# Kernel optimization log

Measured on AMD Instinct MI355X. Metric: run time of the kernel, lower is better.

Reference implementation:

```python
import jax, jax.numpy as jnp
import numpy as np

B = 65536
IN1, IN2 = 384, 128
GRU1, GRU2, NLEVELS = 384, 16, 256


def gru_step(x, h, kernel, rkernel, bias):
    """Single Keras GRU (reset_after=True) step. Gate order: z, r, h.
    kernel: [in, 3u], rkernel: [u, 3u], bias: [2, 3u] (input bias, recurrent bias)."""
    u = h.shape[-1]
    xi = x @ kernel + bias[0]          # [B, 3u]
    hr = h @ rkernel + bias[1]         # [B, 3u]
    xz, xr, xh = xi[:, :u], xi[:, u:2 * u], xi[:, 2 * u:]
    hz, hrr, hh = hr[:, :u], hr[:, u:2 * u], hr[:, 2 * u:]
    z = jax.nn.sigmoid(xz + hz)
    r = jax.nn.sigmoid(xr + hrr)
    hcand = jnp.tanh(xh + r * hh)
    return z * h + (1.0 - z) * hcand


def setup_inputs() -> dict:
    key = jax.random.key(0)
    ks = jax.random.split(key, 14)
    s = lambda fan: 1.0 / np.sqrt(fan)
    return {
        "x1": jax.random.normal(ks[0], (B, IN1), jnp.float32),
        "x2": jax.random.normal(ks[1], (B, IN2), jnp.float32),
        "gru1_kernel": jax.random.normal(ks[2], (IN1 + IN2, 3 * GRU1), jnp.float32) * s(IN1 + IN2),
        "gru1_rkernel": jax.random.normal(ks[3], (GRU1, 3 * GRU1), jnp.float32) * s(GRU1),
        "gru1_bias": jax.random.normal(ks[4], (2, 3 * GRU1), jnp.float32) * 0.01,
        "gru2_kernel": jax.random.normal(ks[5], (GRU1, 3 * GRU2), jnp.float32) * s(GRU1),
        "gru2_rkernel": jax.random.normal(ks[6], (GRU2, 3 * GRU2), jnp.float32) * s(GRU2),
        "gru2_bias": jax.random.normal(ks[7], (2, 3 * GRU2), jnp.float32) * 0.01,
        "fc_w1": jax.random.normal(ks[8], (GRU2, NLEVELS), jnp.float32) * s(GRU2),
        "fc_b1": jax.random.normal(ks[9], (NLEVELS,), jnp.float32) * 0.01,
        "fc_w2": jax.random.normal(ks[10], (GRU2, NLEVELS), jnp.float32) * s(GRU2),
        "fc_b2": jax.random.normal(ks[11], (NLEVELS,), jnp.float32) * 0.01,
        "fc_g1": jax.random.normal(ks[12], (NLEVELS,), jnp.float32),
        "fc_g2": jax.random.normal(ks[13], (NLEVELS,), jnp.float32),
    }


def reference(x1, x2, gru1_kernel, gru1_rkernel, gru1_bias,
              gru2_kernel, gru2_rkernel, gru2_bias,
              fc_w1, fc_b1, fc_w2, fc_b2, fc_g1, fc_g2):
    e = jnp.concatenate([x1, x2], axis=-1)                      # [B, 512]
    h1 = gru_step(e, jnp.zeros((e.shape[0], GRU1), e.dtype),
                  gru1_kernel, gru1_rkernel, gru1_bias)         # [B, 384]
    h2 = gru_step(h1, jnp.zeros((e.shape[0], GRU2), e.dtype),
                  gru2_kernel, gru2_rkernel, gru2_bias)         # [B, 16]
    # DualFC (LPCNet): weighted sum of two tanh branches
    d = fc_g1 * jnp.tanh(h2 @ fc_w1 + fc_b1) + fc_g2 * jnp.tanh(h2 @ fc_w2 + fc_b2)
    return jax.nn.softmax(d, axis=-1)                           # [B, 256]
```

## Files before the change

### kernel.cpp

```cpp
#include <hip/hip_runtime.h>

typedef unsigned short u16;
typedef unsigned int   u32;
typedef float f32x4 __attribute__((ext_vector_type(4)));
typedef short s16x8 __attribute__((ext_vector_type(8)));

#define NB    65536
#define K1    512
#define N1    1152
#define G1D   384
#define K2    384
#define G2D   16
#define NL    256

__device__ inline u16 f2bf(float f) {
  u32 u = __float_as_uint(f);
  u += 0x7fffu + ((u >> 16) & 1u);
  return (u16)(u >> 16);
}
__device__ inline float bf2f(u16 h) { return __uint_as_float(((u32)h) << 16); }
__device__ inline float sigmoidf_(float x) { return 1.0f / (1.0f + __expf(-x)); }
__device__ inline float tanhf_(float x) {
  float e = __expf(2.0f * fabsf(x));
  float t = 1.0f - 2.0f / (e + 1.0f);
  return copysignf(t, x);
}

__device__ inline void gld16(const u16* g, u16* l) {
  __builtin_amdgcn_global_load_lds(
      (const __attribute__((address_space(1))) void*)g,
      (__attribute__((address_space(3))) void*)l, 16, 0, 0);
}

__global__ void prep_a(const float* __restrict__ x1, const float* __restrict__ x2,
                       u16* __restrict__ Abf) {
  int t = blockIdx.x * 256 + threadIdx.x;
  int i = t * 8;
  int row = i >> 9, col = i & 511;
  const float* src = (col < 384) ? (x1 + row * 384 + col) : (x2 + row * 128 + (col - 384));
  float4 v0 = ((const float4*)src)[0];
  float4 v1 = ((const float4*)src)[1];
  union { uint4 v; u16 u[8]; } o;
  o.u[0] = f2bf(v0.x); o.u[1] = f2bf(v0.y); o.u[2] = f2bf(v0.z); o.u[3] = f2bf(v0.w);
  o.u[4] = f2bf(v1.x); o.u[5] = f2bf(v1.y); o.u[6] = f2bf(v1.z); o.u[7] = f2bf(v1.w);
  *(uint4*)(Abf + i) = o.v;
}

__global__ __launch_bounds__(256) void prep_wt1(const float* __restrict__ w,
                                                u16* __restrict__ wt) {
  __shared__ float tile[64][65];
  const int nt = blockIdx.x * 64;
  const int kt = blockIdx.y * 64;
  const int tr = threadIdx.x >> 4;
  const int tc = (threadIdx.x & 15) * 4;
#pragma unroll
  for (int p = 0; p < 4; p++) {
    int k = kt + p * 16 + tr;
    float4 v = *(const float4*)(w + (long)k * N1 + nt + tc);
    tile[p * 16 + tr][tc + 0] = v.x;
    tile[p * 16 + tr][tc + 1] = v.y;
    tile[p * 16 + tr][tc + 2] = v.z;
    tile[p * 16 + tr][tc + 3] = v.w;
  }
  __syncthreads();
  const int nl = threadIdx.x >> 3;
  const int kc = (threadIdx.x & 7) * 8;
#pragma unroll
  for (int p = 0; p < 2; p++) {
    int n = nl + p * 32;
    union { uint4 v; u16 u[8]; } o;
#pragma unroll
    for (int j = 0; j < 8; j++) o.u[j] = f2bf(tile[kc + j][n]);
    *(uint4*)(wt + (long)(nt + n) * K1 + kt + kc) = o.v;
  }
}

__global__ void prep_wt(const float* __restrict__ w, u16* __restrict__ wt, int K, int N) {
  int n = blockIdx.x;
  int k0 = threadIdx.x * 8;
  if (k0 >= K) return;
  union { uint4 v; u16 u[8]; } o;
#pragma unroll
  for (int j = 0; j < 8; j++) o.u[j] = f2bf(w[(k0 + j) * N + n]);
  *(uint4*)(wt + n * K + k0) = o.v;
}

__global__ __launch_bounds__(256) void gemm1gate(const u16* __restrict__ A,
                                                 const u16* __restrict__ Bt,
                                                 const float* __restrict__ bias,
                                                 u16* __restrict__ H1) {
  __shared__ u16 As[128 * 32];
  __shared__ u16 Bs[3][64 * 32];
  const int tid = threadIdx.x;
  const int wave = tid >> 6, lane = tid & 63;
  const int quad = lane >> 4, l16 = lane & 15;

  const int id = blockIdx.x;
  const int xcd = id & 7;
  const int s = id >> 3;
  const int sd6 = s / 6;
  const int ublk = s - sd6 * 6;
  const int mbase = (xcd * 64 + sd6) * 128;
  const int ucbase = ublk * 64;

  const int wm = (wave & 1) * 64, wu = (wave >> 1) * 32;

  f32x4 acc[3][4][2];
#pragma unroll
  for (int g = 0; g < 3; g++)
#pragma unroll
    for (int i = 0; i < 4; i++)
#pragma unroll
      for (int j = 0; j < 2; j++)
#pragma unroll
        for (int r = 0; r < 4; r++) acc[g][i][j][r] = 0.0f;

  const int r0 = tid >> 2;
  const int kcg = ((tid & 3) ^ ((r0 >> 1) & 3)) * 8;
  const u16* Aptr = A + (long)(mbase + r0) * K1 + kcg;
  const u16* Bptr0 = Bt + (long)(0 * G1D + ucbase + r0) * K1 + kcg;
  const u16* Bptr1 = Bt + (long)(1 * G1D + ucbase + r0) * K1 + kcg;
  const u16* Bptr2 = Bt + (long)(2 * G1D + ucbase + r0) * K1 + kcg;
  u16* ldsA0 = As + tid * 8;
  u16* ldsA1 = As + 2048 + tid * 8;
  u16* ldsB0 = Bs[0] + tid * 8;
  u16* ldsB1 = Bs[1] + tid * 8;
  u16* ldsB2 = Bs[2] + tid * 8;

  const s16x8* apf[4];
#pragma unroll
  for (int i = 0; i < 4; i++) {
    int ra = wm + i * 16 + l16;
    apf[i] = (const s16x8*)(As + ra * 32 + ((quad ^ ((ra >> 1) & 3)) << 3));
  }
  const s16x8* bpf[3][2];
#pragma unroll
  for (int g = 0; g < 3; g++)
#pragma unroll
    for (int j = 0; j < 2; j++) {
      int rb = wu + j * 16 + l16;
      bpf[g][j] = (const s16x8*)(Bs[g] + rb * 32 + ((quad ^ ((rb >> 1) & 3)) << 3));
    }

  for (int k0 = 0; k0 < K1; k0 += 32) {
    __syncthreads();
    gld16(Aptr + k0, ldsA0);
    gld16(Aptr + 64 * K1 + k0, ldsA1);
    gld16(Bptr0 + k0, ldsB0);
    gld16(Bptr1 + k0, ldsB1);
    gld16(Bptr2 + k0, ldsB2);
    __syncthreads();
    s16x8 af[4];
#pragma unroll
    for (int i = 0; i < 4; i++) af[i] = *apf[i];
#pragma unroll
    for (int g = 0; g < 3; g++) {
      s16x8 bf0 = *bpf[g][0];
      s16x8 bf1 = *bpf[g][1];
#pragma unroll
      for (int mi = 0; mi < 4; mi++) {
        acc[g][mi][0] = __builtin_amdgcn_mfma_f32_16x16x32_bf16(af[mi], bf0, acc[g][mi][0], 0, 0, 0);
        acc[g][mi][1] = __builtin_amdgcn_mfma_f32_16x16x32_bf16(af[mi], bf1, acc[g][mi][1], 0, 0, 0);
      }
    }
  }

#pragma unroll
  for (int j = 0; j < 2; j++) {
    int u = ucbase + wu + j * 16 + l16;
    float bz = bias[u] + bias[1152 + u];
    float br = bias[384 + u] + bias[1536 + u];
    float bh0 = bias[768 + u];
    float bh1 = bias[1920 + u];
#pragma unroll
    for (int mi = 0; mi < 4; mi++) {
#pragma unroll
      for (int rr = 0; rr < 4; rr++) {
        int row = mbase + wm + mi * 16 + quad * 4 + rr;
        float z  = sigmoidf_(acc[0][mi][j][rr] + bz);
        float rg = sigmoidf_(acc[1][mi][j][rr] + br);
        float hc = tanhf_(acc[2][mi][j][rr] + bh0 + rg * bh1);
        H1[(long)row * G1D + u] = f2bf((1.0f - z) * hc);
      }
    }
  }
}

__global__ __launch_bounds__(256) void gemm2fc(const u16* __restrict__ H1b,
                                               const u16* __restrict__ W2t,
                                               const float* __restrict__ bias2,
                                               const float* __restrict__ w1,
                                               const float* __restrict__ fb1,
                                               const float* __restrict__ w2,
                                               const float* __restrict__ fb2,
                                               const float* __restrict__ g1,
                                               const float* __restrict__ g2,
                                               float* __restrict__ out) {
  __shared__ u16 As[128 * 32];
  __shared__ u16 Bs[48 * 32];
  __shared__ float h2s[128 * 17];
  const int tid = threadIdx.x;
  const int wave = tid >> 6, lane = tid & 63;
  const int quad = lane >> 4, l16 = lane & 15;
  const int mbase = blockIdx.x * 128;

  f32x4 acc[2][3];
#pragma unroll
  for (int i = 0; i < 2; i++)
#pragma unroll
    for (int j = 0; j < 3; j++)
#pragma unroll
      for (int r = 0; r < 4; r++) acc[i][j][r] = 0.0f;

  const int r0 = tid >> 2, kc = (tid & 3) * 8;
  const u16* Aptr = H1b + (long)(mbase + r0) * K2 + kc;

  for (int k0 = 0; k0 < K2; k0 += 32) {
    uint4 a0 = *(const uint4*)(Aptr + k0);
    uint4 a1 = *(const uint4*)(Aptr + 64 * K2 + k0);
    uint4 bv;
    if (tid < 192) bv = *(const uint4*)(W2t + r0 * K2 + k0 + kc);
    __syncthreads();
    *(uint4*)(&As[r0 * 32 + kc]) = a0;
    *(uint4*)(&As[(64 + r0) * 32 + kc]) = a1;
    if (tid < 192) *(uint4*)(&Bs[r0 * 32 + kc]) = bv;
    __syncthreads();
    s16x8 af[2], bfr[3];
#pragma unroll
    for (int mi = 0; mi < 2; mi++)
      af[mi] = *(const s16x8*)(&As[(wave * 32 + mi * 16 + l16) * 32 + quad * 8]);
#pragma unroll
    for (int ni = 0; ni < 3; ni++)
      bfr[ni] = *(const s16x8*)(&Bs[(ni * 16 + l16) * 32 + quad * 8]);
#pragma unroll
    for (int mi = 0; mi < 2; mi++)
#pragma unroll
      for (int ni = 0; ni < 3; ni++)
        acc[mi][ni] = __builtin_amdgcn_mfma_f32_16x16x32_bf16(af[mi], bfr[ni], acc[mi][ni], 0, 0, 0);
  }

  {
    const int u = l16;
    const float b0z = bias2[u],      b1z = bias2[48 + u];
    const float b0r = bias2[16 + u], b1r = bias2[64 + u];
    const float b0h = bias2[32 + u], b1h = bias2[80 + u];
#pragma unroll
    for (int mi = 0; mi < 2; mi++) {
#pragma unroll
      for (int rr = 0; rr < 4; rr++) {
        int row_l = wave * 32 + mi * 16 + quad * 4 + rr;
        float z  = sigmoidf_(acc[mi][0][rr] + b0z + b1z);
        float rg = sigmoidf_(acc[mi][1][rr] + b0r + b1r);
        float hc = tanhf_(acc[mi][2][rr] + b0h + rg * b1h);
        h2s[row_l * 17 + u] = (1.0f - z) * hc;
      }
    }
  }
  __syncthreads();

#pragma unroll 1
  for (int r = 0; r < 32; r++) {
    int row_l = wave * 32 + r;
    float h[16];
#pragma unroll
    for (int uu = 0; uu < 16; uu++) h[uu] = h2s[row_l * 17 + uu];
    float e[4];
    float mx = -1e30f;
#pragma unroll
    for (int i = 0; i < 4; i++) {
      int c = i * 64 + lane;
      float a1 = fb1[c], a2 = fb2[c];
#pragma unroll
      for (int uu = 0; uu < 16; uu++) {
        a1 = fmaf(h[uu], w1[uu * 256 + c], a1);
        a2 = fmaf(h[uu], w2[uu * 256 + c], a2);
      }
      float d = g1[c] * tanhf_(a1) + g2[c] * tanhf_(a2);
      e[i] = d;
      mx = fmaxf(mx, d);
    }
#pragma unroll
    for (int off = 32; off >= 1; off >>= 1) mx = fmaxf(mx, __shfl_xor(mx, off, 64));
    float sum = 0.0f;
#pragma unroll
    for (int i = 0; i < 4; i++) { e[i] = __expf(e[i] - mx); sum += e[i]; }
#pragma unroll
    for (int off = 32; off >= 1; off >>= 1) sum += __shfl_xor(sum, off, 64);
    float inv = 1.0f / sum;
    float* orow = out + (long)(mbase + row_l) * NL;
#pragma unroll
    for (int i = 0; i < 4; i++) orow[i * 64 + lane] = e[i] * inv;
  }
}

extern "C" void kernel_launch(void* const* d_in, const int* in_sizes, int n_in,
                              void* d_out, int out_size, void* d_ws, size_t ws_size,
                              hipStream_t stream) {
  const float* x1   = (const float*)d_in[0];
  const float* x2   = (const float*)d_in[1];
  const float* w1k  = (const float*)d_in[2];
  const float* b1g  = (const float*)d_in[4];
  const float* w2k  = (const float*)d_in[5];
  const float* b2g  = (const float*)d_in[7];
  const float* fcw1 = (const float*)d_in[8];
  const float* fcb1 = (const float*)d_in[9];
  const float* fcw2 = (const float*)d_in[10];
  const float* fcb2 = (const float*)d_in[11];
  const float* fcg1 = (const float*)d_in[12];
  const float* fcg2 = (const float*)d_in[13];
  float* out = (float*)d_out;

  char* ws = (char*)d_ws;
  u16* Abf = (u16*)(ws + 0);
  u16* W1t = (u16*)(ws + 67108864);
  u16* H1  = (u16*)(ws + 68288512);
  u16* W2t = (u16*)(ws + 118620160);

  hipLaunchKernelGGL(prep_a, dim3(16384), dim3(256), 0, stream, x1, x2, Abf);
  hipLaunchKernelGGL(prep_wt1, dim3(18, 8), dim3(256), 0, stream, w1k, W1t);
  hipLaunchKernelGGL(prep_wt, dim3(48), dim3(64), 0, stream, w2k, W2t, 384, 48);
  hipLaunchKernelGGL(gemm1gate, dim3(3072), dim3(256), 0, stream, Abf, W1t, b1g, H1);
  hipLaunchKernelGGL(gemm2fc, dim3(512), dim3(256), 0, stream, H1, W2t, b2g,
                     fcw1, fcb1, fcw2, fcb2, fcg1, fcg2, out);
}
```

Baseline: 382.3 us.

## Load GRU1 weights directly into registers from a fragment-packed layout and quad-buffer A tiles

The weight transpose kernel now writes the bf16 GRU1 weights in an MFMA-fragment-ordered layout, so each lane can load its B fragments straight from global memory into registers without staging them in LDS. The A tile moves to a 4-deep LDS ring with loads issued two steps ahead, explicit vmcnt waits and a single barrier per K step in place of two syncthreads. MFMA issue priority is also raised. This targets LDS traffic and synchronisation stalls in the main loop, in exchange for more live registers, fragile hand-counted waitcnt values and redundant B reads from global/L2 across waves.

```diff
diff --git a/kernel.cpp b/kernel.cpp
--- a/kernel.cpp
+++ b/kernel.cpp
@@ -50,12 +50,12 @@
                                                 u16* __restrict__ wt) {
   __shared__ float tile[64][65];
   const int nt = blockIdx.x * 64;
-  const int kt = blockIdx.y * 64;
+  const int ktb = blockIdx.y * 64;
   const int tr = threadIdx.x >> 4;
   const int tc = (threadIdx.x & 15) * 4;
 #pragma unroll
   for (int p = 0; p < 4; p++) {
-    int k = kt + p * 16 + tr;
+    int k = ktb + p * 16 + tr;
     float4 v = *(const float4*)(w + (long)k * N1 + nt + tc);
     tile[p * 16 + tr][tc + 0] = v.x;
     tile[p * 16 + tr][tc + 1] = v.y;
@@ -68,10 +68,17 @@
 #pragma unroll
   for (int p = 0; p < 2; p++) {
     int n = nl + p * 32;
+    int c = nt + n;
+    int g = c / 384;
+    int urem = c - g * 384;
+    int ut = urem >> 4, u16c = urem & 15;
+    int k0 = ktb + kc;
+    int kt = k0 >> 5, qd = (k0 >> 3) & 3;
     union { uint4 v; u16 u[8]; } o;
 #pragma unroll
     for (int j = 0; j < 8; j++) o.u[j] = f2bf(tile[kc + j][n]);
-    *(uint4*)(wt + (long)(nt + n) * K1 + kt + kc) = o.v;
+    long off = ((long)((g * 24 + ut) * 16 + kt) * 64 + qd * 16 + u16c) * 8;
+    *(uint4*)(wt + off) = o.v;
   }
 }
 
@@ -85,12 +92,11 @@
   *(uint4*)(wt + n * K + k0) = o.v;
 }
 
-__global__ __launch_bounds__(256) void gemm1gate(const u16* __restrict__ A,
-                                                 const u16* __restrict__ Bt,
-                                                 const float* __restrict__ bias,
-                                                 u16* __restrict__ H1) {
-  __shared__ u16 As[128 * 32];
-  __shared__ u16 Bs[3][64 * 32];
+__global__ __launch_bounds__(256, 2) void gemm1gate(const u16* __restrict__ A,
+                                                    const u16* __restrict__ Bf,
+                                                    const float* __restrict__ bias,
+                                                    u16* __restrict__ H1) {
+  __shared__ u16 As[4][128 * 32];
   const int tid = threadIdx.x;
   const int wave = tid >> 6, lane = tid & 63;
   const int quad = lane >> 4, l16 = lane & 15;
@@ -104,6 +110,7 @@
   const int ucbase = ublk * 64;
 
   const int wm = (wave & 1) * 64, wu = (wave >> 1) * 32;
+  const int ut0 = ublk * 4 + (wave >> 1) * 2;
 
   f32x4 acc[3][4][2];
 #pragma unroll
@@ -117,52 +124,73 @@
 
   const int r0 = tid >> 2;
   const int kcg = ((tid & 3) ^ ((r0 >> 1) & 3)) * 8;
-  const u16* Aptr = A + (long)(mbase + r0) * K1 + kcg;
-  const u16* Bptr0 = Bt + (long)(0 * G1D + ucbase + r0) * K1 + kcg;
-  const u16* Bptr1 = Bt + (long)(1 * G1D + ucbase + r0) * K1 + kcg;
-  const u16* Bptr2 = Bt + (long)(2 * G1D + ucbase + r0) * K1 + kcg;
-  u16* ldsA0 = As + tid * 8;
-  u16* ldsA1 = As + 2048 + tid * 8;
-  u16* ldsB0 = Bs[0] + tid * 8;
-  u16* ldsB1 = Bs[1] + tid * 8;
-  u16* ldsB2 = Bs[2] + tid * 8;
-
-  const s16x8* apf[4];
+  const u16* Aptr  = A + (long)(mbase + r0) * K1 + kcg;
+  const u16* Aptr2 = Aptr + 64 * K1;
+  const u16* Bl = Bf + lane * 8;
+
+  int aoff[4];
 #pragma unroll
   for (int i = 0; i < 4; i++) {
     int ra = wm + i * 16 + l16;
-    apf[i] = (const s16x8*)(As + ra * 32 + ((quad ^ ((ra >> 1) & 3)) << 3));
-  }
-  const s16x8* bpf[3][2];
+    aoff[i] = ra * 32 + ((quad ^ ((ra >> 1) & 3)) << 3);
+  }
+
+  s16x8 bn[3][2];
 #pragma unroll
   for (int g = 0; g < 3; g++)
 #pragma unroll
-    for (int j = 0; j < 2; j++) {
-      int rb = wu + j * 16 + l16;
-      bpf[g][j] = (const s16x8*)(Bs[g] + rb * 32 + ((quad ^ ((rb >> 1) & 3)) << 3));
-    }
-
-  for (int k0 = 0; k0 < K1; k0 += 32) {
-    __syncthreads();
-    gld16(Aptr + k0, ldsA0);
-    gld16(Aptr + 64 * K1 + k0, ldsA1);
-    gld16(Bptr0 + k0, ldsB0);
-    gld16(Bptr1 + k0, ldsB1);
-    gld16(Bptr2 + k0, ldsB2);
-    __syncthreads();
+    for (int j = 0; j < 2; j++)
+      bn[g][j] = *(const s16x8*)(Bl + (long)((g * 24 + ut0 + j) * 16 + 0) * 512);
+  asm volatile("" ::: "memory");
+  gld16(Aptr,       &As[0][tid * 8]);
+  gld16(Aptr2,      &As[0][2048 + tid * 8]);
+  gld16(Aptr + 32,  &As[1][tid * 8]);
+  gld16(Aptr2 + 32, &As[1][2048 + tid * 8]);
+
+#pragma unroll
+  for (int t = 0; t < 16; ++t) {
+    s16x8 bcur[3][2];
+#pragma unroll
+    for (int g = 0; g < 3; g++)
+#pragma unroll
+      for (int j = 0; j < 2; j++) bcur[g][j] = bn[g][j];
+
+    if (t < 15) {
+      const int tb = t + 1;
+#pragma unroll
+      for (int g = 0; g < 3; g++)
+#pragma unroll
+        for (int j = 0; j < 2; j++)
+          bn[g][j] = *(const s16x8*)(Bl + (long)((g * 24 + ut0 + j) * 16 + tb) * 512);
+    }
+    asm volatile("" ::: "memory");
+    if (t < 14) {
+      const int ta = t + 2;
+      gld16(Aptr  + ta * 32, &As[(t + 2) & 3][tid * 8]);
+      gld16(Aptr2 + ta * 32, &As[(t + 2) & 3][2048 + tid * 8]);
+    }
+    if (t == 0)       asm volatile("s_waitcnt vmcnt(10)" ::: "memory");
+    else if (t < 14)  asm volatile("s_waitcnt vmcnt(16)" ::: "memory");
+    else if (t == 14) asm volatile("s_waitcnt vmcnt(14)" ::: "memory");
+    else              asm volatile("s_waitcnt vmcnt(6)"  ::: "memory");
+    __builtin_amdgcn_s_barrier();
+    asm volatile("" ::: "memory");
+
+    const u16* buf = &As[t & 3][0];
     s16x8 af[4];
 #pragma unroll
-    for (int i = 0; i < 4; i++) af[i] = *apf[i];
+    for (int i = 0; i < 4; i++) af[i] = *(const s16x8*)(buf + aoff[i]);
+
+    __builtin_amdgcn_s_setprio(1);
 #pragma unroll
     for (int g = 0; g < 3; g++) {
-      s16x8 bf0 = *bpf[g][0];
-      s16x8 bf1 = *bpf[g][1];
 #pragma unroll
       for (int mi = 0; mi < 4; mi++) {
-        acc[g][mi][0] = __builtin_amdgcn_mfma_f32_16x16x32_bf16(af[mi], bf0, acc[g][mi][0], 0, 0, 0);
-        acc[g][mi][1] = __builtin_amdgcn_mfma_f32_16x16x32_bf16(af[mi], bf1, acc[g][mi][1], 0, 0, 0);
+        acc[g][mi][0] = __builtin_amdgcn_mfma_f32_16x16x32_bf16(af[mi], bcur[g][0], acc[g][mi][0], 0, 0, 0);
+        acc[g][mi][1] = __builtin_amdgcn_mfma_f32_16x16x32_bf16(af[mi], bcur[g][1], acc[g][mi][1], 0, 0, 0);
       }
     }
+    __builtin_amdgcn_s_setprio(0);
   }
 
 #pragma unroll
```

After: 364.9 us. -4.6%, faster.
